# Optimization experiments

Measured on AMD Instinct MI355X. Metric: run time of the kernel, lower is better.

## Reference

```python
import jax, jax.numpy as jnp
import numpy as np

T = 1024
D = 2048
H = 16
NOPE = 128
ROPE = 64
VDIM = 128
QKD = NOPE + ROPE
Q_LORA = 768
KV_LORA = 512
IH = 32          # indexer heads
ID = 128         # indexer head dim (== fp8 quant group size)
TOPK = 256       # indexer top-k sparse selection
E = 8
MOE_K = 2
F = 1024
SH_F = 1024
EPS = 1e-6
FP8_MAX = 448.0
ROUTED_SCALE = 2.5
NEG = jnp.float32(-1e30)


def rms_norm(x, w):
    return x * jax.lax.rsqrt(jnp.mean(jnp.square(x), -1, keepdims=True) + EPS) * w


def layer_norm(x, w, b):
    m = jnp.mean(x, -1, keepdims=True)
    v = jnp.mean(jnp.square(x - m), -1, keepdims=True)
    return (x - m) * jax.lax.rsqrt(v + EPS) * w + b


def rope(x, positions, rope_dim):
    # interleaved (GPT-J style, as DeepSeek MLA uses is_neox_style=False); x: [T, Hx, rope_dim]
    half = rope_dim // 2
    inv_freq = 1.0 / (10000.0 ** (jnp.arange(half, dtype=jnp.float32) / half))
    ang = positions.astype(jnp.float32)[:, None] * inv_freq        # [T, half]
    cos = jnp.cos(ang)[:, None, :]
    sin = jnp.sin(ang)[:, None, :]
    x1, x2 = x[..., ::2], x[..., 1::2]
    return jnp.stack([x1 * cos - x2 * sin, x2 * cos + x1 * sin], -1).reshape(x.shape)


def fp8_quant(x):
    # per-token-group (group = last dim = 128) fp8 e4m3 quant with ue8m0 (power-of-2) scales
    amax = jnp.max(jnp.abs(x), -1, keepdims=True)
    scale = jnp.exp2(jnp.ceil(jnp.log2(jnp.maximum(amax / FP8_MAX, 1e-10))))
    q = jnp.clip(x / scale, -FP8_MAX, FP8_MAX).astype(jnp.float8_e4m3fn).astype(jnp.float32)
    return q, scale


def _forward(positions, hidden_states, residual, input_ln_w, post_ln_w, w_qkv_a, q_a_ln_w,
             w_q_b, kv_a_ln_w, w_kv_b, w_o, w_idx_q_b, w_idx_k, idx_k_ln_w, idx_k_ln_b,
             w_idx_weights, w_gate, w_moe_gate, w_moe_up, w_moe_down, w_sh_gate, w_sh_up, w_sh_down):
    t = hidden_states.shape[0]
    # fused_add_rms_norm
    resid = hidden_states + residual
    hs = rms_norm(resid, input_ln_w)

    # fused qkv_a projection and splits
    qkv = hs @ w_qkv_a                                   # [t, Q_LORA + KV_LORA + ROPE]
    q_c = rms_norm(qkv[:, :Q_LORA], q_a_ln_w)
    kv_c = qkv[:, Q_LORA:Q_LORA + KV_LORA]
    k_pe = qkv[:, Q_LORA + KV_LORA:]
    q = (q_c @ w_q_b).reshape(t, H, QKD)
    kv_c_n = rms_norm(kv_c, kv_a_ln_w)
    q_pe = rope(q[..., NOPE:], positions, ROPE)
    k_pe = rope(k_pe[:, None, :], positions, ROPE)       # [t, 1, ROPE]
    q = jnp.concatenate([q[..., :NOPE], q_pe], -1)

    # lightning indexer: RoPE-split q/k, fp8 per-token-group quant, weighted ReLU scores, top-k
    iq = (q_c @ w_idx_q_b).reshape(t, IH, ID)
    ik = layer_norm(hs @ w_idx_k, idx_k_ln_w, idx_k_ln_b)  # [t, ID]
    iq_pe = rope(iq[..., :ROPE], positions, ROPE)
    ik_pe = rope(ik[:, None, :ROPE], positions, ROPE)[:, 0]
    iq = jnp.concatenate([iq_pe, iq[..., ROPE:]], -1)
    ik = jnp.concatenate([ik_pe, ik[:, ROPE:]], -1)
    iq_fp8, iq_scale = fp8_quant(iq.reshape(t * IH, ID))
    iq_fp8 = iq_fp8.reshape(t, IH, ID)
    iq_scale = iq_scale.reshape(t, IH)
    ik_fp8, ik_scale = fp8_quant(ik)
    # weights_proj * q_scale * softmax_scale * n_heads^-0.5
    iw = (hs @ w_idx_weights) * iq_scale * (ID ** -0.5) * (IH ** -0.5)
    logits = jnp.einsum('thd,sd->ths', iq_fp8, ik_fp8) * ik_scale[:, 0][None, None, :]
    causal = jnp.arange(t)[:, None] >= jnp.arange(t)[None, :]
    scores = jnp.einsum('ths,th->ts', jax.nn.relu(logits), iw)
    scores = jnp.where(causal, scores, NEG)
    topk_idx = jax.lax.top_k(scores, TOPK)[1]            # [t, TOPK]
    sel = jnp.zeros((t, t), bool).at[jnp.arange(t)[:, None], topk_idx].set(True)
    mask = causal & sel

    # MLA attention restricted to indexer-selected tokens
    kv = (kv_c_n @ w_kv_b).reshape(t, H, NOPE + VDIM)
    k = jnp.concatenate([kv[..., :NOPE], jnp.broadcast_to(k_pe, (t, H, ROPE))], -1)
    att = jnp.einsum('thd,shd->hts', q, k) * (QKD ** -0.5)
    att = jnp.where(mask[None], att, NEG)
    p = jax.nn.softmax(att, -1)
    o = jnp.einsum('hts,shv->thv', p, kv[..., NOPE:]).reshape(t, H * VDIM)

    # o_proj + fused_add_rms_norm
    resid = o @ w_o + resid
    hs = rms_norm(resid, post_ln_w)

    # MoE: sigmoid gate, top-k normalized, routed_scaling, SwiGLU experts + shared expert
    gate = jax.nn.sigmoid(hs @ w_gate)                   # [t, E]
    tw, ti = jax.lax.top_k(gate, MOE_K)
    tw = tw / jnp.sum(tw, -1, keepdims=True)
    wfull = jnp.zeros((t, E)).at[jnp.arange(t)[:, None], ti].set(tw) * ROUTED_SCALE
    hmid = jax.nn.silu(jnp.einsum('td,edf->tef', hs, w_moe_gate)) * jnp.einsum('td,edf->tef', hs, w_moe_up)
    routed = jnp.einsum('tef,efd,te->td', hmid, w_moe_down, wfull)
    shared = (jax.nn.silu(hs @ w_sh_gate) * (hs @ w_sh_up)) @ w_sh_down
    return routed + shared, resid


def setup_inputs() -> dict:
    key = jax.random.key(0)
    ks = jax.random.split(key, 16)
    s = 0.02
    return {
        'positions': jnp.arange(T, dtype=jnp.int32),
        'hidden_states': jax.random.normal(ks[0], (T, D), jnp.float32),
        'residual': jax.random.normal(ks[1], (T, D), jnp.float32),
        'input_ln_w': jnp.ones((D,), jnp.float32),
        'post_ln_w': jnp.ones((D,), jnp.float32),
        'w_qkv_a': s * jax.random.normal(ks[2], (D, Q_LORA + KV_LORA + ROPE), jnp.float32),
        'q_a_ln_w': jnp.ones((Q_LORA,), jnp.float32),
        'w_q_b': s * jax.random.normal(ks[3], (Q_LORA, H * QKD), jnp.float32),
        'kv_a_ln_w': jnp.ones((KV_LORA,), jnp.float32),
        'w_kv_b': s * jax.random.normal(ks[4], (KV_LORA, H * (NOPE + VDIM)), jnp.float32),
        'w_o': s * jax.random.normal(ks[5], (H * VDIM, D), jnp.float32),
        'w_idx_q_b': s * jax.random.normal(ks[6], (Q_LORA, IH * ID), jnp.float32),
        'w_idx_k': s * jax.random.normal(ks[7], (D, ID), jnp.float32),
        'idx_k_ln_w': jnp.ones((ID,), jnp.float32),
        'idx_k_ln_b': jnp.zeros((ID,), jnp.float32),
        'w_idx_weights': s * jax.random.normal(ks[8], (D, IH), jnp.float32),
        'w_gate': s * jax.random.normal(ks[9], (D, E), jnp.float32),
        'w_moe_gate': s * jax.random.normal(ks[10], (E, D, F), jnp.float32),
        'w_moe_up': s * jax.random.normal(ks[11], (E, D, F), jnp.float32),
        'w_moe_down': s * jax.random.normal(ks[12], (E, F, D), jnp.float32),
        'w_sh_gate': s * jax.random.normal(ks[13], (D, SH_F), jnp.float32),
        'w_sh_up': s * jax.random.normal(ks[14], (D, SH_F), jnp.float32),
        'w_sh_down': s * jax.random.normal(ks[15], (SH_F, D), jnp.float32),
    }


def reference(positions, hidden_states, residual, input_ln_w, post_ln_w, w_qkv_a, q_a_ln_w,
              w_q_b, kv_a_ln_w, w_kv_b, w_o, w_idx_q_b, w_idx_k, idx_k_ln_w, idx_k_ln_b,
              w_idx_weights, w_gate, w_moe_gate, w_moe_up, w_moe_down, w_sh_gate, w_sh_up, w_sh_down):
    return _forward(positions, hidden_states, residual, input_ln_w, post_ln_w, w_qkv_a, q_a_ln_w,
                    w_q_b, kv_a_ln_w, w_kv_b, w_o, w_idx_q_b, w_idx_k, idx_k_ln_w, idx_k_ln_b,
                    w_idx_weights, w_gate, w_moe_gate, w_moe_up, w_moe_down, w_sh_gate, w_sh_up, w_sh_down)
```

## Files before the change

### kernel.cpp

```cpp
#include <hip/hip_runtime.h>

namespace {
constexpr int kT = 1024, kD = 2048, kH = 16, kNOPE = 128, kROPE = 64, kVD = 128, kQKD = 192;
constexpr int kQL = 768, kKVL = 512, kIH = 32, kID = 128, kTOPK = 256, kE = 8, kF = 1024;
constexpr int kQKV_N = kQL + kKVL + kROPE;
constexpr int kQKV_NP = 1408;
}

typedef __attribute__((ext_vector_type(4))) float floatx4;
typedef __attribute__((ext_vector_type(8))) short short8;
typedef unsigned short u16;

__device__ __forceinline__ float wsum(float v) {
#pragma unroll
  for (int o = 32; o; o >>= 1) v += __shfl_xor(v, o, 64);
  return v;
}
__device__ __forceinline__ float wmax64(float v) {
#pragma unroll
  for (int o = 32; o; o >>= 1) v = fmaxf(v, __shfl_xor(v, o, 64));
  return v;
}
__device__ __forceinline__ int wsum_i(int v) {
#pragma unroll
  for (int o = 32; o; o >>= 1) v += __shfl_xor(v, o, 64);
  return v;
}
__device__ __forceinline__ float bsum256(float v, float* red) {
  v = wsum(v);
  if ((threadIdx.x & 63) == 0) red[threadIdx.x >> 6] = v;
  __syncthreads();
  float t = red[0] + red[1] + red[2] + red[3];
  __syncthreads();
  return t;
}
__device__ __forceinline__ unsigned sortkey(float f) {
  unsigned b = __float_as_uint(f);
  return (b & 0x80000000u) ? ~b : (b | 0x80000000u);
}
__device__ __forceinline__ float pow2ceil(float z) {
  unsigned b = __float_as_uint(z);
  if ((b & 0x7FFFFFu) == 0) return z;
  return __uint_as_float((((b >> 23) & 0xFFu) + 1u) << 23);
}
__device__ __forceinline__ float fp8q(float x) {
  float ax = fabsf(x);
  float q;
  if (ax < 0.015625f) {
    q = rintf(ax * 512.0f) * 0.001953125f;
  } else {
    unsigned b = __float_as_uint(ax);
    int e = (int)((b >> 23) & 0xFF) - 127;
    float quant = __uint_as_float((unsigned)(e - 3 + 127) << 23);
    float rq    = __uint_as_float((unsigned)(127 - (e - 3)) << 23);
    q = rintf(ax * rq) * quant;
  }
  return copysignf(q, x);
}
__device__ __forceinline__ u16 f2bf(float x) {
  unsigned u = __float_as_uint(x);
  u += 0x7FFFu + ((u >> 16) & 1u);
  return (u16)(u >> 16);
}
__device__ __forceinline__ float bf2f(u16 h) { return __uint_as_float((unsigned)h << 16); }

__device__ __forceinline__ void gld_lds16(const void* g, void* l) {
  __builtin_amdgcn_global_load_lds(
      (const __attribute__((address_space(1))) unsigned int*)(unsigned long long)g,
      (__attribute__((address_space(3))) unsigned int*)(unsigned int)(unsigned long long)l,
      16, 0, 0);
}
__device__ __forceinline__ void stage_tile(const u16* g, size_t strideUs, u16* tile, int wave, int lane) {
  int r = lane >> 2, c = lane & 3;
  const u16* gp = g + (size_t)(wave * 32 + r) * strideUs + c * 8;
  gld_lds16(gp, tile + (wave * 32) * 32);
  gld_lds16(gp + (size_t)16 * strideUs, tile + (wave * 32 + 16) * 32);
}

__global__ __launch_bounds__(256) void k_transpose_w(const float* __restrict__ in, u16* __restrict__ hi,
                                                     u16* __restrict__ lo, int K, int N, int Npad) {
  __shared__ float tile[32][33];
  int n0 = blockIdx.x * 32, k0 = blockIdx.y * 32;
  const float* ip = in + (size_t)blockIdx.z * K * N;
  u16* hp = hi + (size_t)blockIdx.z * Npad * K;
  u16* lp = lo ? lo + (size_t)blockIdx.z * Npad * K : nullptr;
  int t = threadIdx.x;
  int r = t >> 3, c4 = (t & 7) << 2;
  if (n0 < N) {
    float4 v = *(const float4*)&ip[(size_t)(k0 + r) * N + n0 + c4];
    tile[r][c4] = v.x; tile[r][c4 + 1] = v.y; tile[r][c4 + 2] = v.z; tile[r][c4 + 3] = v.w;
  } else {
    tile[r][c4] = 0.f; tile[r][c4 + 1] = 0.f; tile[r][c4 + 2] = 0.f; tile[r][c4 + 3] = 0.f;
  }
  __syncthreads();
  int n = t >> 3, kq = (t & 7) << 2;
  ushort4 h4, l4;
#pragma unroll
  for (int j = 0; j < 4; j++) {
    float f = tile[kq + j][n];
    u16 h = f2bf(f);
    ((u16*)&h4)[j] = h;
    ((u16*)&l4)[j] = f2bf(f - bf2f(h));
  }
  *(ushort4*)&hp[(size_t)(n0 + n) * K + k0 + kq] = h4;
  if (lp) *(ushort4*)&lp[(size_t)(n0 + n) * K + k0 + kq] = l4;
}


__global__ __launch_bounds__(256) void k_gemm_bt(const u16* __restrict__ A, const u16* __restrict__ BT,
                                                 float* __restrict__ C, const float* __restrict__ addend,
                                                 int M, int N, int K) {
  __shared__ __align__(16) u16 As[128 * 32];
  __shared__ __align__(16) u16 Bs[128 * 32];
  int tid = threadIdx.x, wave = tid >> 6, lane = tid & 63;
  int bm = blockIdx.y * 128, bn = blockIdx.x * 128;
  int wy = (wave >> 1) * 64, wx = (wave & 1) * 64;
  int lm = lane & 15, lk = lane >> 4;
  const u16* Ab = A + (size_t)bm * K;
  const u16* Bb = BT + (size_t)bn * K;
  floatx4 acc[4][4] = {};
  for (int k0 = 0; k0 < K; k0 += 32) {
    stage_tile(Ab + k0, K, As, wave, lane);
    stage_tile(Bb + k0, K, Bs, wave, lane);
    __syncthreads();
    short8 af[4], bfr[4];
#pragma unroll
    for (int mt = 0; mt < 4; mt++) af[mt] = *(short8*)&As[(wy + mt * 16 + lm) * 32 + lk * 8];
#pragma unroll
    for (int nt = 0; nt < 4; nt++) bfr[nt] = *(short8*)&Bs[(wx + nt * 16 + lm) * 32 + lk * 8];
#pragma unroll
    for (int mt = 0; mt < 4; mt++)
#pragma unroll
      for (int nt = 0; nt < 4; nt++)
        acc[mt][nt] = __builtin_amdgcn_mfma_f32_16x16x32_bf16(af[mt], bfr[nt], acc[mt][nt], 0, 0, 0);
    __syncthreads();
  }
#pragma unroll
  for (int mt = 0; mt < 4; mt++)
#pragma unroll
    for (int nt = 0; nt < 4; nt++)
#pragma unroll
      for (int r = 0; r < 4; r++) {
        int m = bm + wy + mt * 16 + lk * 4 + r;
        int n = bn + wx + nt * 16 + lm;
        float v = acc[mt][nt][r];
        if (addend) v += addend[(size_t)m * N + n];
        C[(size_t)m * N + n] = v;
      }
}

__global__ __launch_bounds__(256) void k_gemm_split(const u16* __restrict__ Ah, const u16* __restrict__ Al,
                                                    const u16* __restrict__ Bh, const u16* __restrict__ Bl,
                                                    float* __restrict__ C, int M, int N, int K) {
  __shared__ __align__(16) u16 Ahs[128 * 32];
  __shared__ __align__(16) u16 Als[128 * 32];
  __shared__ __align__(16) u16 Bhs[128 * 32];
  __shared__ __align__(16) u16 Bls[128 * 32];
  int tid = threadIdx.x, wave = tid >> 6, lane = tid & 63;
  int bm = blockIdx.y * 128, bn = blockIdx.x * 128;
  int wy = (wave >> 1) * 64, wx = (wave & 1) * 64;
  int lm = lane & 15, lk = lane >> 4;
  floatx4 acc[4][4] = {};
  for (int k0 = 0; k0 < K; k0 += 32) {
    stage_tile(Ah + (size_t)bm * K + k0, K, Ahs, wave, lane);
    stage_tile(Al + (size_t)bm * K + k0, K, Als, wave, lane);
    stage_tile(Bh + (size_t)bn * K + k0, K, Bhs, wave, lane);
    stage_tile(Bl + (size_t)bn * K + k0, K, Bls, wave, lane);
    __syncthreads();
    short8 ah[4], al[4], bh[4], bl[4];
#pragma unroll
    for (int mt = 0; mt < 4; mt++) { ah[mt] = *(short8*)&Ahs[(wy + mt * 16 + lm) * 32 + lk * 8];
                                     al[mt] = *(short8*)&Als[(wy + mt * 16 + lm) * 32 + lk * 8]; }
#pragma unroll
    for (int nt = 0; nt < 4; nt++) { bh[nt] = *(short8*)&Bhs[(wx + nt * 16 + lm) * 32 + lk * 8];
                                     bl[nt] = *(short8*)&Bls[(wx + nt * 16 + lm) * 32 + lk * 8]; }
#pragma unroll
    for (int mt = 0; mt < 4; mt++)
#pragma unroll
      for (int nt = 0; nt < 4; nt++) {
        floatx4 a = acc[mt][nt];
        a = __builtin_amdgcn_mfma_f32_16x16x32_bf16(al[mt], bh[nt], a, 0, 0, 0);
        a = __builtin_amdgcn_mfma_f32_16x16x32_bf16(ah[mt], bl[nt], a, 0, 0, 0);
        a = __builtin_amdgcn_mfma_f32_16x16x32_bf16(ah[mt], bh[nt], a, 0, 0, 0);
        acc[mt][nt] = a;
      }
    __syncthreads();
  }
#pragma unroll
  for (int mt = 0; mt < 4; mt++)
#pragma unroll
    for (int nt = 0; nt < 4; nt++)
#pragma unroll
      for (int r = 0; r < 4; r++) {
        int m = bm + wy + mt * 16 + lk * 4 + r;
        int n = bn + wx + nt * 16 + lm;
        if (n < N) C[(size_t)m * N + n] = acc[mt][nt][r];
      }
}

__global__ __launch_bounds__(256) void k_dual_bt(const u16* __restrict__ A, const u16* __restrict__ GT,
                                                 const u16* __restrict__ UT, u16* __restrict__ out,
                                                 const int* __restrict__ toki, const int* __restrict__ cnt,
                                                 int M, int N, int K) {
  int e = blockIdx.z;
  int n_rows = toki ? cnt[e] : M;
  int bm = blockIdx.y * 128;
  if (bm >= n_rows) return;
  int bn = blockIdx.x * 128;
  const int* tk = toki ? (toki + e * kT) : nullptr;
  const u16* Gb = GT + (size_t)e * N * K + (size_t)bn * K;
  const u16* Ub = UT + (size_t)e * N * K + (size_t)bn * K;
  u16* oP = out + (size_t)e * kT * N;
  __shared__ __align__(16) u16 As[128 * 32];
  __shared__ __align__(16) u16 Gs[128 * 32];
  __shared__ __align__(16) u16 Us[128 * 32];
  int tid = threadIdx.x, wave = tid >> 6, lane = tid & 63;
  int wy = (wave >> 1) * 64, wx = (wave & 1) * 64;
  int lm = lane & 15, lk = lane >> 4;
  int r = lane >> 2, c = lane & 3;
  int r0 = bm + wave * 32 + r, r1 = r0 + 16;
  size_t arow0 = tk ? (size_t)((r0 < n_rows) ? tk[r0] : 0) : (size_t)r0;
  size_t arow1 = tk ? (size_t)((r1 < n_rows) ? tk[r1] : 0) : (size_t)r1;
  floatx4 ag[4][4] = {}, au[4][4] = {};
  for (int k0 = 0; k0 < K; k0 += 32) {
    gld_lds16(A + arow0 * K + k0 + c * 8, As + (wave * 32) * 32);
    gld_lds16(A + arow1 * K + k0 + c * 8, As + (wave * 32 + 16) * 32);
    stage_tile(Gb + k0, K, Gs, wave, lane);
    stage_tile(Ub + k0, K, Us, wave, lane);
    __syncthreads();
    short8 af[4], gf[4], uf[4];
#pragma unroll
    for (int mt = 0; mt < 4; mt++) af[mt] = *(short8*)&As[(wy + mt * 16 + lm) * 32 + lk * 8];
#pragma unroll
    for (int nt = 0; nt < 4; nt++) { gf[nt] = *(short8*)&Gs[(wx + nt * 16 + lm) * 32 + lk * 8];
                                     uf[nt] = *(short8*)&Us[(wx + nt * 16 + lm) * 32 + lk * 8]; }
#pragma unroll
    for (int mt = 0; mt < 4; mt++)
#pragma unroll
      for (int nt = 0; nt < 4; nt++) {
        ag[mt][nt] = __builtin_amdgcn_mfma_f32_16x16x32_bf16(af[mt], gf[nt], ag[mt][nt], 0, 0, 0);
        au[mt][nt] = __builtin_amdgcn_mfma_f32_16x16x32_bf16(af[mt], uf[nt], au[mt][nt], 0, 0, 0);
      }
    __syncthreads();
  }
#pragma unroll
  for (int mt = 0; mt < 4; mt++)
#pragma unroll
    for (int nt = 0; nt < 4; nt++)
#pragma unroll
      for (int r2 = 0; r2 < 4; r2++) {
        int gm = bm + wy + mt * 16 + lk * 4 + r2;
        if (gm >= n_rows) continue;
        int n = bn + wx + nt * 16 + lm;
        float gv = ag[mt][nt][r2], uv = au[mt][nt][r2];
        oP[(size_t)gm * N + n] = f2bf(gv * (1.0f / (1.0f + expf(-gv))) * uv);
      }
}

__global__ __launch_bounds__(256) void k_down_bt(const u16* __restrict__ hmid, const u16* __restrict__ DT,
                                                 const int* __restrict__ toki, const float* __restrict__ tokw,
                                                 const int* __restrict__ cnt, float* __restrict__ out) {
  int e = blockIdx.z;
  int n_rows = cnt[e];
  int bm = blockIdx.y * 128;
  if (bm >= n_rows) return;
  int bn = blockIdx.x * 128;
  const u16* Ab = hmid + (size_t)e * kT * kF + (size_t)bm * kF;
  const u16* Bb = DT + (size_t)e * kD * kF + (size_t)bn * kF;
  __shared__ __align__(16) u16 As[128 * 32];
  __shared__ __align__(16) u16 Bs[128 * 32];
  int tid = threadIdx.x, wave = tid >> 6, lane = tid & 63;
  int wy = (wave >> 1) * 64, wx = (wave & 1) * 64;
  int lm = lane & 15, lk = lane >> 4;
  floatx4 acc[4][4] = {};
  for (int k0 = 0; k0 < kF; k0 += 32) {
    stage_tile(Ab + k0, kF, As, wave, lane);
    stage_tile(Bb + k0, kF, Bs, wave, lane);
    __syncthreads();
    short8 af[4], bfr[4];
#pragma unroll
    for (int mt = 0; mt < 4; mt++) af[mt] = *(short8*)&As[(wy + mt * 16 + lm) * 32 + lk * 8];
#pragma unroll
    for (int nt = 0; nt < 4; nt++) bfr[nt] = *(short8*)&Bs[(wx + nt * 16 + lm) * 32 + lk * 8];
#pragma unroll
    for (int mt = 0; mt < 4; mt++)
#pragma unroll
      for (int nt = 0; nt < 4; nt++)
        acc[mt][nt] = __builtin_amdgcn_mfma_f32_16x16x32_bf16(af[mt], bfr[nt], acc[mt][nt], 0, 0, 0);
    __syncthreads();
  }
#pragma unroll
  for (int mt = 0; mt < 4; mt++)
#pragma unroll
    for (int r = 0; r < 4; r++) {
      int gm = bm + wy + mt * 16 + lk * 4 + r;
      if (gm >= n_rows) continue;
      int tt = toki[e * kT + gm];
      float w = tokw[e * kT + gm];
#pragma unroll
      for (int nt = 0; nt < 4; nt++) {
        int n = bn + wx + nt * 16 + lm;
        atomicAdd(&out[(size_t)tt * kD + n], w * acc[mt][nt][r]);
      }
    }
}

__global__ __launch_bounds__(256) void k_attn_mfma(const float* __restrict__ q, const float* __restrict__ kv,
                                                   const float* __restrict__ kpe,
                                                   const unsigned long long* __restrict__ mbits,
                                                   u16* __restrict__ o) {
  __shared__ __align__(16) u16 Ks[64 * 200];
  __shared__ __align__(16) u16 Vs[128 * 72];
  __shared__ __align__(16) u16 Ps[4 * 16 * 72];
  int h = blockIdx.y;
  int qb = gridDim.x - 1 - blockIdx.x;
  int qbase = qb * 64;
  int tid = threadIdx.x;
  int wave = tid >> 6, lane = tid & 63;
  int lm = lane & 15, lk = lane >> 4;
  short8 qf[6];
  {
    const float* qrow = q + ((size_t)(qbase + wave * 16 + lm) * kH + h) * kQKD;
#pragma unroll
    for (int ks = 0; ks < 6; ks++) {
      const float4 a0 = *(const float4*)&qrow[ks * 32 + lk * 8];
      const float4 a1 = *(const float4*)&qrow[ks * 32 + lk * 8 + 4];
      short8 f;
      f[0] = (short)f2bf(a0.x); f[1] = (short)f2bf(a0.y); f[2] = (short)f2bf(a0.z); f[3] = (short)f2bf(a0.w);
      f[4] = (short)f2bf(a1.x); f[5] = (short)f2bf(a1.y); f[6] = (short)f2bf(a1.z); f[7] = (short)f2bf(a1.w);
      qf[ks] = f;
    }
  }
  float m_r[4] = {-1e30f, -1e30f, -1e30f, -1e30f};
  float l_r[4] = {};
  floatx4 Oacc[8] = {};
  int sr = tid >> 2, sj = tid & 3;
  int nch = qb + 1;
  for (int ch = 0; ch < nch; ch++) {
    int s0 = ch << 6;
    __syncthreads();
    {
      const float* kvrow = kv + ((size_t)(s0 + sr) * kH + h) * 256;
      const float* kprow = kpe + (size_t)(s0 + sr) * 64;
#pragma unroll
      for (int i = 0; i < 12; i++) {
        int c4 = (i << 2) + sj;
        float4 v4 = (c4 < 32) ? *(const float4*)&kvrow[c4 * 4] : *(const float4*)&kprow[(c4 - 32) * 4];
        ushort4 p; p.x = f2bf(v4.x); p.y = f2bf(v4.y); p.z = f2bf(v4.z); p.w = f2bf(v4.w);
        *(ushort4*)&Ks[sr * 200 + c4 * 4] = p;
      }
      const float* vrow = kvrow + 128;
#pragma unroll
      for (int i = 0; i < 8; i++) {
        int c4 = (i << 2) + sj;
        float4 v4 = *(const float4*)&vrow[c4 * 4];
        Vs[(c4 * 4 + 0) * 72 + sr] = f2bf(v4.x);
        Vs[(c4 * 4 + 1) * 72 + sr] = f2bf(v4.y);
        Vs[(c4 * 4 + 2) * 72 + sr] = f2bf(v4.z);
        Vs[(c4 * 4 + 3) * 72 + sr] = f2bf(v4.w);
      }
    }
    __syncthreads();
    floatx4 sacc[4] = {};
#pragma unroll
    for (int ks = 0; ks < 6; ks++) {
      short8 kf[4];
#pragma unroll
      for (int nt = 0; nt < 4; nt++) kf[nt] = *(short8*)&Ks[(nt * 16 + lm) * 200 + ks * 32 + lk * 8];
#pragma unroll
      for (int nt = 0; nt < 4; nt++)
        sacc[nt] = __builtin_amdgcn_mfma_f32_16x16x32_bf16(qf[ks], kf[nt], sacc[nt], 0, 0, 0);
    }
    unsigned long long mw[4];
#pragma unroll
    for (int r = 0; r < 4; r++) mw[r] = mbits[(size_t)(qbase + wave * 16 + lk * 4 + r) * 16 + ch];
    float mx[4] = {-1e30f, -1e30f, -1e30f, -1e30f};
#pragma unroll
    for (int nt = 0; nt < 4; nt++)
#pragma unroll
      for (int r = 0; r < 4; r++) {
        int sel = (int)((mw[r] >> (nt * 16 + lm)) & 1ull);
        float sv = sel ? sacc[nt][r] * 0.07216878364870323f : -1e30f;
        sacc[nt][r] = sv;
        mx[r] = fmaxf(mx[r], sv);
      }
#pragma unroll
    for (int off = 1; off < 16; off <<= 1)
#pragma unroll
      for (int r = 0; r < 4; r++) mx[r] = fmaxf(mx[r], __shfl_xor(mx[r], off, 64));
    float al[4], psum[4] = {};
#pragma unroll
    for (int r = 0; r < 4; r++) {
      float mnew = fmaxf(m_r[r], mx[r]);
      al[r] = __expf(m_r[r] - mnew);
      m_r[r] = mnew;
    }
#pragma unroll
    for (int nt = 0; nt < 4; nt++)
#pragma unroll
      for (int r = 0; r < 4; r++) {
        float p = (sacc[nt][r] > -0.9e30f) ? __expf(sacc[nt][r] - m_r[r]) : 0.0f;
        psum[r] += p;
        Ps[wave * 1152 + (lk * 4 + r) * 72 + nt * 16 + lm] = f2bf(p);
      }
#pragma unroll
    for (int off = 1; off < 16; off <<= 1)
#pragma unroll
      for (int r = 0; r < 4; r++) psum[r] += __shfl_xor(psum[r], off, 64);
#pragma unroll
    for (int r = 0; r < 4; r++) l_r[r] = l_r[r] * al[r] + psum[r];
#pragma unroll
    for (int nv = 0; nv < 8; nv++)
#pragma unroll
      for (int r = 0; r < 4; r++) Oacc[nv][r] *= al[r];
    short8 pf[2];
#pragma unroll
    for (int k2 = 0; k2 < 2; k2++) pf[k2] = *(short8*)&Ps[wave * 1152 + lm * 72 + k2 * 32 + lk * 8];
#pragma unroll
    for (int k2 = 0; k2 < 2; k2++)
#pragma unroll
      for (int nv = 0; nv < 8; nv++) {
        short8 vf = *(short8*)&Vs[(nv * 16 + lm) * 72 + k2 * 32 + lk * 8];
        Oacc[nv] = __builtin_amdgcn_mfma_f32_16x16x32_bf16(pf[k2], vf, Oacc[nv], 0, 0, 0);
      }
  }
  float invl[4];
#pragma unroll
  for (int r = 0; r < 4; r++) invl[r] = 1.0f / l_r[r];
#pragma unroll
  for (int nv = 0; nv < 8; nv++)
#pragma unroll
    for (int r = 0; r < 4; r++) {
      int t_row = qbase + wave * 16 + lk * 4 + r;
      o[((size_t)t_row * kH + h) * kVD + nv * 16 + lm] = f2bf(Oacc[nv][r] * invl[r]);
    }
}

__global__ __launch_bounds__(256) void k_add_rms(const float* __restrict__ h, const float* __restrict__ r,
                                                 const float* __restrict__ w, float* __restrict__ resid,
                                                 float* __restrict__ out, u16* __restrict__ oh,
                                                 u16* __restrict__ ol) {
  __shared__ float row[kD];
  __shared__ float red[4];
  int t = blockIdx.x;
  size_t base = (size_t)t * kD;
  float ss = 0.f;
  for (int c = threadIdx.x; c < kD; c += 256) {
    float v = h[base + c] + r[base + c];
    row[c] = v; resid[base + c] = v; ss += v * v;
  }
  float tot = bsum256(ss, red);
  float inv = 1.0f / sqrtf(tot * (1.0f / kD) + 1e-6f);
  for (int c = threadIdx.x; c < kD; c += 256) {
    float v = row[c] * inv * w[c];
    out[base + c] = v;
    u16 hb = f2bf(v);
    oh[base + c] = hb;
    ol[base + c] = f2bf(v - bf2f(hb));
  }
}

__global__ __launch_bounds__(256) void k_rms_rows(const float* __restrict__ in, int stride, int off,
                                                  const float* __restrict__ w, float* __restrict__ outf,
                                                  u16* __restrict__ oh, u16* __restrict__ ol, int cols) {
  __shared__ float row[kD];
  __shared__ float red[4];
  int t = blockIdx.x;
  const float* x = in + (size_t)t * stride + off;
  float ss = 0.f;
  for (int c = threadIdx.x; c < cols; c += 256) { float v = x[c]; row[c] = v; ss += v * v; }
  float tot = bsum256(ss, red);
  float inv = 1.0f / sqrtf(tot / (float)cols + 1e-6f);
  for (int c = threadIdx.x; c < cols; c += 256) {
    float v = row[c] * inv * w[c];
    if (outf) outf[(size_t)t * cols + c] = v;
    if (oh) {
      u16 hb = f2bf(v);
      oh[(size_t)t * cols + c] = hb;
      if (ol) ol[(size_t)t * cols + c] = f2bf(v - bf2f(hb));
    }
  }
}

__global__ __launch_bounds__(256) void k_iw_fused(const float* __restrict__ hs, const float* __restrict__ w,
                                                  const float* __restrict__ iqsc, float* __restrict__ out) {
  __shared__ float red[4][32];
  int t = blockIdx.x;
  int tid = threadIdx.x;
  int h = tid & 31, g = tid >> 5;
  const float* hrow = hs + (size_t)t * kD;
  float acc = 0.f;
#pragma unroll 4
  for (int d = g; d < kD; d += 8) acc += hrow[d] * w[(size_t)d * kIH + h];
  acc += __shfl_xor(acc, 32, 64);
  int wave = tid >> 6, lane = tid & 63;
  if (lane < 32) red[wave][lane] = acc;
  __syncthreads();
  if (tid < 32) {
    float v = red[0][tid] + red[1][tid] + red[2][tid] + red[3][tid];
    out[t * kIH + tid] = v * iqsc[t * kIH + tid] * 0.08838834764831845f * 0.17677669529663687f;
  }
}

__global__ __launch_bounds__(256) void k_rope_q(float* __restrict__ q, const int* __restrict__ pos) {
  int t = blockIdx.x;
  float p = (float)pos[t];
  for (int idx = threadIdx.x; idx < kH * 32; idx += 256) {
    int h = idx >> 5, j = idx & 31;
    float invf = 1.0f / powf(10000.0f, (float)j * 0.03125f);
    float ang = p * invf; float s, c; sincosf(ang, &s, &c);
    size_t base = ((size_t)t * kH + h) * kQKD + kNOPE + 2 * j;
    float x1 = q[base], x2 = q[base + 1];
    q[base] = x1 * c - x2 * s;
    q[base + 1] = x2 * c + x1 * s;
  }
}

__global__ __launch_bounds__(256) void k_rope_iq(float* __restrict__ iq, const int* __restrict__ pos) {
  int t = blockIdx.x;
  float p = (float)pos[t];
  for (int idx = threadIdx.x; idx < kIH * 32; idx += 256) {
    int h = idx >> 5, j = idx & 31;
    float invf = 1.0f / powf(10000.0f, (float)j * 0.03125f);
    float ang = p * invf; float s, c; sincosf(ang, &s, &c);
    size_t base = ((size_t)t * kIH + h) * kID + 2 * j;
    float x1 = iq[base], x2 = iq[base + 1];
    iq[base] = x1 * c - x2 * s;
    iq[base + 1] = x2 * c + x1 * s;
  }
}

__global__ __launch_bounds__(64) void k_rope_kpe(const float* __restrict__ qkv, const int* __restrict__ pos,
                                                 float* __restrict__ kpe) {
  int t = blockIdx.x; int j = threadIdx.x;
  if (j >= 32) return;
  float p = (float)pos[t];
  float invf = 1.0f / powf(10000.0f, (float)j * 0.03125f);
  float ang = p * invf; float s, c; sincosf(ang, &s, &c);
  const float* src = qkv + (size_t)t * kQKV_N + kQL + kKVL;
  float x1 = src[2 * j], x2 = src[2 * j + 1];
  kpe[(size_t)t * 64 + 2 * j] = x1 * c - x2 * s;
  kpe[(size_t)t * 64 + 2 * j + 1] = x2 * c + x1 * s;
}

__global__ __launch_bounds__(64) void k_quant_rows(const float* __restrict__ x, u16* __restrict__ outq,
                                                   float* __restrict__ scales) {
  int row = blockIdx.x;
  const float* p = x + (size_t)row * kID;
  int l = threadIdx.x;
  float v0 = p[2 * l], v1 = p[2 * l + 1];
  float am = wmax64(fmaxf(fabsf(v0), fabsf(v1)));
  float scale = pow2ceil(fmaxf(am / 448.0f, 1e-10f));
  float inv = 1.0f / scale;
  float q0 = fp8q(fminf(fmaxf(v0 * inv, -448.f), 448.f));
  float q1 = fp8q(fminf(fmaxf(v1 * inv, -448.f), 448.f));
  ushort2 pk; pk.x = f2bf(q0); pk.y = f2bf(q1);
  *(ushort2*)&outq[(size_t)row * kID + 2 * l] = pk;
  if (l == 0) scales[row] = scale;
}

__global__ __launch_bounds__(64) void k_ik_process(const float* __restrict__ raw, const float* __restrict__ w,
                                                   const float* __restrict__ b, const int* __restrict__ pos,
                                                   u16* __restrict__ outq, float* __restrict__ scales) {
  int t = blockIdx.x; int l = threadIdx.x;
  const float* x = raw + (size_t)t * kID;
  float x0 = x[2 * l], x1 = x[2 * l + 1];
  float mean = wsum(x0 + x1) * (1.0f / 128.0f);
  float d0 = x0 - mean, d1 = x1 - mean;
  float var = wsum(d0 * d0 + d1 * d1) * (1.0f / 128.0f);
  float inv = 1.0f / sqrtf(var + 1e-6f);
  float y0 = d0 * inv * w[2 * l] + b[2 * l];
  float y1 = d1 * inv * w[2 * l + 1] + b[2 * l + 1];
  if (l < 32) {
    float p = (float)pos[t];
    float invf = 1.0f / powf(10000.0f, (float)l * 0.03125f);
    float ang = p * invf; float sn, cs; sincosf(ang, &sn, &cs);
    float r0 = y0 * cs - y1 * sn, r1 = y1 * cs + y0 * sn;
    y0 = r0; y1 = r1;
  }
  float am = wmax64(fmaxf(fabsf(y0), fabsf(y1)));
  float scale = pow2ceil(fmaxf(am / 448.0f, 1e-10f));
  float is = 1.0f / scale;
  float q0 = fp8q(fminf(fmaxf(y0 * is, -448.f), 448.f));
  float q1 = fp8q(fminf(fmaxf(y1 * is, -448.f), 448.f));
  ushort2 pk; pk.x = f2bf(q0); pk.y = f2bf(q1);
  *(ushort2*)&outq[(size_t)t * kID + 2 * l] = pk;
  if (l == 0) scales[t] = scale;
}

__global__ __launch_bounds__(256) void k_scores_mfma(const u16* __restrict__ iq, const u16* __restrict__ ik,
                                                     const float* __restrict__ iksc, const float* __restrict__ iw,
                                                     float* __restrict__ scores) {
  int tb = blockIdx.y * 4;
  int bn = blockIdx.x * 128;
  if (bn > tb + 3) return;
  __shared__ __align__(16) u16 As[128 * 32];
  __shared__ __align__(16) u16 Bs[128 * 32];
  int tid = threadIdx.x, wave = tid >> 6, lane = tid & 63;
  int wy = (wave >> 1) * 64, wx = (wave & 1) * 64;
  int lm = lane & 15, lk = lane >> 4;
  const u16* Ab = iq + (size_t)(tb * kIH) * kID;
  const u16* Bb = ik + (size_t)bn * kID;
  floatx4 acc[4][4] = {};
  for (int k0 = 0; k0 < kID; k0 += 32) {
    stage_tile(Ab + k0, kID, As, wave, lane);
    stage_tile(Bb + k0, kID, Bs, wave, lane);
    __syncthreads();
    short8 af[4], bfr[4];
#pragma unroll
    for (int mt = 0; mt < 4; mt++) af[mt] = *(short8*)&As[(wy + mt * 16 + lm) * 32 + lk * 8];
#pragma unroll
    for (int nt = 0; nt < 4; nt++) bfr[nt] = *(short8*)&Bs[(wx + nt * 16 + lm) * 32 + lk * 8];
#pragma unroll
    for (int mt = 0; mt < 4; mt++)
#pragma unroll
      for (int nt = 0; nt < 4; nt++)
        acc[mt][nt] = __builtin_amdgcn_mfma_f32_16x16x32_bf16(af[mt], bfr[nt], acc[mt][nt], 0, 0, 0);
    __syncthreads();
  }
  float scv[4];
#pragma unroll
  for (int nt = 0; nt < 4; nt++) scv[nt] = iksc[bn + wx + nt * 16 + lm];
  float iwv[4][4];
#pragma unroll
  for (int mt = 0; mt < 4; mt++)
#pragma unroll
    for (int r = 0; r < 4; r++)
      iwv[mt][r] = iw[(tb + (wy >> 5) + (mt >> 1)) * kIH + (mt & 1) * 16 + lk * 4 + r];
#pragma unroll
  for (int tp = 0; tp < 2; tp++) {
    int tglob = tb + (wy >> 5) + tp;
#pragma unroll
    for (int nt = 0; nt < 4; nt++) {
      float v = 0.f;
#pragma unroll
      for (int mh = 0; mh < 2; mh++) {
        int mt = tp * 2 + mh;
#pragma unroll
        for (int r = 0; r < 4; r++)
          v += fmaxf(acc[mt][nt][r] * scv[nt], 0.f) * iwv[mt][r];
      }
      v += __shfl_xor(v, 16, 64);
      v += __shfl_xor(v, 32, 64);
      if (lk == 0) scores[(size_t)tglob * kT + bn + wx + nt * 16 + lm] = v;
    }
  }
}

__global__ __launch_bounds__(64) void k_topk(const float* __restrict__ scores, unsigned long long* __restrict__ mbits) {
  int t = blockIdx.x; int l = threadIdx.x;
  __shared__ unsigned short tmp[64];
  unsigned long long* mrow = mbits + (size_t)t * 16;
  if (t < kTOPK) {
    if (l < 16) {
      int lo = l * 64, hi = lo + 63;
      unsigned long long bits;
      if (hi <= t) bits = ~0ull;
      else if (lo > t) bits = 0ull;
      else bits = (1ull << (t - lo + 1)) - 1ull;
      mrow[l] = bits;
    }
    return;
  }
  unsigned key[16];
  const float* srow = scores + (size_t)t * kT;
#pragma unroll
  for (int i = 0; i < 16; i++) {
    int s = l * 16 + i;
    key[i] = (s <= t) ? sortkey(srow[s]) : 0u;
  }
  unsigned prefix = 0; int remaining = kTOPK;
  for (int bit = 31; bit >= 0; bit--) {
    unsigned himask = 0xFFFFFFFFu << bit;
    unsigned cmp = prefix | (1u << bit);
    int c = 0;
#pragma unroll
    for (int i = 0; i < 16; i++) c += ((key[i] & himask) == cmp) ? 1 : 0;
    c = wsum_i(c);
    if (c >= remaining) prefix = cmp; else remaining -= c;
  }
  int ceq = 0, cgt = 0;
#pragma unroll
  for (int i = 0; i < 16; i++) { ceq += (key[i] == prefix) ? 1 : 0; cgt += (key[i] > prefix) ? 1 : 0; }
  int v = ceq;
#pragma unroll
  for (int o = 1; o < 64; o <<= 1) { int u = __shfl_up(v, o, 64); if (l >= o) v += u; }
  int rank = v - ceq;
  int need = kTOPK - wsum_i(cgt);
  unsigned short mybits = 0;
#pragma unroll
  for (int i = 0; i < 16; i++) {
    int sel;
    if (key[i] > prefix) sel = 1;
    else if (key[i] == prefix) { sel = (rank < need) ? 1 : 0; rank++; }
    else sel = 0;
    mybits |= (unsigned short)(sel << i);
  }
  tmp[l] = mybits;
  __syncthreads();
  if (l < 16) {
    mrow[l] = (unsigned long long)tmp[4 * l] | ((unsigned long long)tmp[4 * l + 1] << 16) |
              ((unsigned long long)tmp[4 * l + 2] << 32) | ((unsigned long long)tmp[4 * l + 3] << 48);
  }
}

__global__ __launch_bounds__(64) void k_route(const float* __restrict__ hs2, const float* __restrict__ wg,
                                              int* __restrict__ cnt, int* __restrict__ toki,
                                              float* __restrict__ tokw) {
  int t = blockIdx.x; int l = threadIdx.x;
  float acc[8] = {};
  for (int d = l; d < kD; d += 64) {
    float hv = hs2[(size_t)t * kD + d];
    const float* wr = wg + (size_t)d * 8;
#pragma unroll
    for (int e = 0; e < 8; e++) acc[e] += hv * wr[e];
  }
#pragma unroll
  for (int e = 0; e < 8; e++) acc[e] = wsum(acc[e]);
  if (l == 0) {
    float g[8];
#pragma unroll
    for (int e = 0; e < 8; e++) g[e] = 1.0f / (1.0f + expf(-acc[e]));
    int i0 = 0;
    for (int e = 1; e < 8; e++) if (g[e] > g[i0]) i0 = e;
    int i1 = (i0 == 0) ? 1 : 0;
    for (int e = 0; e < 8; e++) if (e != i0 && g[e] > g[i1]) i1 = e;
    float ssum = g[i0] + g[i1];
    float w0 = g[i0] / ssum * 2.5f, w1 = g[i1] / ssum * 2.5f;
    int s0 = atomicAdd(&cnt[i0], 1); toki[i0 * kT + s0] = t; tokw[i0 * kT + s0] = w0;
    int s1 = atomicAdd(&cnt[i1], 1); toki[i1 * kT + s1] = t; tokw[i1 * kT + s1] = w1;
  }
}

extern "C" void kernel_launch(void* const* d_in, const int* in_sizes, int n_in,
                              void* d_out, int out_size, void* d_ws, size_t ws_size,
                              hipStream_t stream) {
  (void)in_sizes; (void)n_in; (void)out_size; (void)ws_size;
  const int*   positions  = (const int*)d_in[0];
  const float* hidden     = (const float*)d_in[1];
  const float* residual   = (const float*)d_in[2];
  const float* input_ln_w = (const float*)d_in[3];
  const float* post_ln_w  = (const float*)d_in[4];
  const float* w_qkv_a    = (const float*)d_in[5];
  const float* q_a_ln_w   = (const float*)d_in[6];
  const float* w_q_b      = (const float*)d_in[7];
  const float* kv_a_ln_w  = (const float*)d_in[8];
  const float* w_kv_b     = (const float*)d_in[9];
  const float* w_o        = (const float*)d_in[10];
  const float* w_idx_q_b  = (const float*)d_in[11];
  const float* w_idx_k    = (const float*)d_in[12];
  const float* idx_k_ln_w = (const float*)d_in[13];
  const float* idx_k_ln_b = (const float*)d_in[14];
  const float* w_idx_w    = (const float*)d_in[15];
  const float* w_gate     = (const float*)d_in[16];
  const float* w_moe_gate = (const float*)d_in[17];
  const float* w_moe_up   = (const float*)d_in[18];
  const float* w_moe_down = (const float*)d_in[19];
  const float* w_sh_gate  = (const float*)d_in[20];
  const float* w_sh_up    = (const float*)d_in[21];
  const float* w_sh_down  = (const float*)d_in[22];

  float* out0 = (float*)d_out;
  float* out1 = out0 + (size_t)kT * kD;

  char* W = (char*)d_ws;
  size_t off = 0;
  auto alloc = [&](size_t bytes) { char* p = W + off; off += (bytes + 255) & ~(size_t)255; return p; };
  float* resid   = (float*)alloc((size_t)kT * kD * 4);
  float* hs      = (float*)alloc((size_t)kT * kD * 4);
  float* qkv     = (float*)alloc((size_t)kT * kQKV_N * 4);
  float* qb      = (float*)alloc((size_t)kT * kH * kQKD * 4);
  float* kvb     = (float*)alloc((size_t)kT * kH * 256 * 4);
  float* iqb     = (float*)alloc((size_t)kT * kIH * kID * 4);
  float* ikraw   = (float*)alloc((size_t)kT * kID * 4);
  float* iksc    = (float*)alloc(kT * 4);
  float* iqsc    = (float*)alloc((size_t)kT * kIH * 4);
  float* iwb     = (float*)alloc((size_t)kT * kIH * 4);
  float* kpe     = (float*)alloc((size_t)kT * kROPE * 4);
  float* scoresb = (float*)alloc((size_t)kT * kT * 4);
  float* hs2     = (float*)alloc((size_t)kT * kD * 4);
  unsigned long long* mbits = (unsigned long long*)alloc((size_t)kT * 16 * 8);
  float* tokw    = (float*)alloc((size_t)kE * kT * 4);
  int*   toki    = (int*)alloc((size_t)kE * kT * 4);
  int*   cnt     = (int*)alloc(64);
  u16* hs_h   = (u16*)alloc((size_t)kT * kD * 2);
  u16* hs_l   = (u16*)alloc((size_t)kT * kD * 2);
  u16* qc_h   = (u16*)alloc((size_t)kT * kQL * 2);
  u16* qc_l   = (u16*)alloc((size_t)kT * kQL * 2);
  u16* kvc_h  = (u16*)alloc((size_t)kT * kKVL * 2);
  u16* o_bf   = (u16*)alloc((size_t)kT * kH * kVD * 2);
  u16* hs2_h  = (u16*)alloc((size_t)kT * kD * 2);
  u16* sg_bf  = (u16*)alloc((size_t)kT * kF * 2);
  u16* hmid_bf= (u16*)alloc((size_t)kE * kT * kF * 2);
  u16* iq_bf  = (u16*)alloc((size_t)kT * kIH * kID * 2);
  u16* ik_bf  = (u16*)alloc((size_t)kT * kID * 2);
  u16* qkvBT_h = (u16*)alloc((size_t)kQKV_NP * kD * 2);
  u16* qkvBT_l = (u16*)alloc((size_t)kQKV_NP * kD * 2);
  u16* qbBT    = (u16*)alloc((size_t)kH * kQKD * kQL * 2);
  u16* kvbBT   = (u16*)alloc((size_t)kH * 256 * kKVL * 2);
  u16* woBT    = (u16*)alloc((size_t)kD * kH * kVD * 2);
  u16* iqBT_h  = (u16*)alloc((size_t)kIH * kID * kQL * 2);
  u16* iqBT_l  = (u16*)alloc((size_t)kIH * kID * kQL * 2);
  u16* ikBT_h  = (u16*)alloc((size_t)kID * kD * 2);
  u16* ikBT_l  = (u16*)alloc((size_t)kID * kD * 2);
  u16* shgBT   = (u16*)alloc((size_t)kF * kD * 2);
  u16* shuBT   = (u16*)alloc((size_t)kF * kD * 2);
  u16* shdBT   = (u16*)alloc((size_t)kD * kF * 2);
  u16* moegBT  = (u16*)alloc((size_t)kE * kF * kD * 2);
  u16* moeuBT  = (u16*)alloc((size_t)kE * kF * kD * 2);
  u16* moedBT  = (u16*)alloc((size_t)kE * kD * kF * 2);

  { dim3 g(kQKV_NP / 32, kD / 32); k_transpose_w<<<g, 256, 0, stream>>>(w_qkv_a, qkvBT_h, qkvBT_l, kD, kQKV_N, kQKV_NP); }
  { dim3 g(kH * kQKD / 32, kQL / 32); k_transpose_w<<<g, 256, 0, stream>>>(w_q_b, qbBT, nullptr, kQL, kH * kQKD, kH * kQKD); }
  { dim3 g(kH * 256 / 32, kKVL / 32); k_transpose_w<<<g, 256, 0, stream>>>(w_kv_b, kvbBT, nullptr, kKVL, kH * 256, kH * 256); }
  { dim3 g(kD / 32, kH * kVD / 32); k_transpose_w<<<g, 256, 0, stream>>>(w_o, woBT, nullptr, kH * kVD, kD, kD); }
  { dim3 g(kIH * kID / 32, kQL / 32); k_transpose_w<<<g, 256, 0, stream>>>(w_idx_q_b, iqBT_h, iqBT_l, kQL, kIH * kID, kIH * kID); }
  { dim3 g(kID / 32, kD / 32); k_transpose_w<<<g, 256, 0, stream>>>(w_idx_k, ikBT_h, ikBT_l, kD, kID, kID); }
  { dim3 g(kF / 32, kD / 32); k_transpose_w<<<g, 256, 0, stream>>>(w_sh_gate, shgBT, nullptr, kD, kF, kF); }
  { dim3 g(kF / 32, kD / 32); k_transpose_w<<<g, 256, 0, stream>>>(w_sh_up, shuBT, nullptr, kD, kF, kF); }
  { dim3 g(kD / 32, kF / 32); k_transpose_w<<<g, 256, 0, stream>>>(w_sh_down, shdBT, nullptr, kF, kD, kD); }
  { dim3 g(kF / 32, kD / 32, kE); k_transpose_w<<<g, 256, 0, stream>>>(w_moe_gate, moegBT, nullptr, kD, kF, kF); }
  { dim3 g(kF / 32, kD / 32, kE); k_transpose_w<<<g, 256, 0, stream>>>(w_moe_up, moeuBT, nullptr, kD, kF, kF); }
  { dim3 g(kD / 32, kF / 32, kE); k_transpose_w<<<g, 256, 0, stream>>>(w_moe_down, moedBT, nullptr, kF, kD, kD); }

  k_add_rms<<<kT, 256, 0, stream>>>(hidden, residual, input_ln_w, resid, hs, hs_h, hs_l);
  { dim3 g(kQKV_NP / 128, kT / 128); k_gemm_split<<<g, 256, 0, stream>>>(hs_h, hs_l, qkvBT_h, qkvBT_l, qkv, kT, kQKV_N, kD); }
  k_rms_rows<<<kT, 256, 0, stream>>>(qkv, kQKV_N, 0, q_a_ln_w, nullptr, qc_h, qc_l, kQL);
  k_rms_rows<<<kT, 256, 0, stream>>>(qkv, kQKV_N, kQL, kv_a_ln_w, nullptr, kvc_h, nullptr, kKVL);
  { dim3 g(kH * kQKD / 128, kT / 128); k_gemm_bt<<<g, 256, 0, stream>>>(qc_h, qbBT, qb, nullptr, kT, kH * kQKD, kQL); }
  { dim3 g(kIH * kID / 128, kT / 128); k_gemm_split<<<g, 256, 0, stream>>>(qc_h, qc_l, iqBT_h, iqBT_l, iqb, kT, kIH * kID, kQL); }
  { dim3 g(kH * 256 / 128, kT / 128); k_gemm_bt<<<g, 256, 0, stream>>>(kvc_h, kvbBT, kvb, nullptr, kT, kH * 256, kKVL); }
  { dim3 g(kID / 128, kT / 128); k_gemm_split<<<g, 256, 0, stream>>>(hs_h, hs_l, ikBT_h, ikBT_l, ikraw, kT, kID, kD); }
  k_rope_q<<<kT, 256, 0, stream>>>(qb, positions);
  k_rope_iq<<<kT, 256, 0, stream>>>(iqb, positions);
  k_rope_kpe<<<kT, 64, 0, stream>>>(qkv, positions, kpe);
  k_quant_rows<<<kT * kIH, 64, 0, stream>>>(iqb, iq_bf, iqsc);
  k_ik_process<<<kT, 64, 0, stream>>>(ikraw, idx_k_ln_w, idx_k_ln_b, positions, ik_bf, iksc);
  k_iw_fused<<<kT, 256, 0, stream>>>(hs, w_idx_w, iqsc, iwb);
  { dim3 g(kT / 128, kT / 4); k_scores_mfma<<<g, 256, 0, stream>>>(iq_bf, ik_bf, iksc, iwb, scoresb); }
  k_topk<<<kT, 64, 0, stream>>>(scoresb, mbits);
  { dim3 g(kT / 64, kH); k_attn_mfma<<<g, 256, 0, stream>>>(qb, kvb, kpe, mbits, o_bf); }
  { dim3 g(kD / 128, kT / 128); k_gemm_bt<<<g, 256, 0, stream>>>(o_bf, woBT, out1, resid, kT, kD, kH * kVD); }
  k_rms_rows<<<kT, 256, 0, stream>>>(out1, kD, 0, post_ln_w, hs2, hs2_h, nullptr, kD);
  hipMemsetAsync(cnt, 0, 8 * sizeof(int), stream);
  k_route<<<kT, 64, 0, stream>>>(hs2, w_gate, cnt, toki, tokw);
  { dim3 g(kF / 128, kT / 128, 1); k_dual_bt<<<g, 256, 0, stream>>>(hs2_h, shgBT, shuBT, sg_bf, nullptr, nullptr, kT, kF, kD); }
  { dim3 g(kD / 128, kT / 128); k_gemm_bt<<<g, 256, 0, stream>>>(sg_bf, shdBT, out0, nullptr, kT, kD, kF); }
  { dim3 g(kF / 128, kT / 128, kE); k_dual_bt<<<g, 256, 0, stream>>>(hs2_h, moegBT, moeuBT, hmid_bf, toki, cnt, kT, kF, kD); }
  { dim3 g(kD / 128, kT / 128, kE); k_down_bt<<<g, 256, 0, stream>>>(hmid_bf, moedBT, toki, tokw, cnt, out0); }
}
```

Before: 1.148 ms.

## Fuse indexer-k projection into qkv_a GEMM and split K four ways

Appends the indexer key weight to the padded qkv_a weight matrix so one GEMM computes both projections. That GEMM is split along K into four chunks writing partial sums to a scratch buffer (aliased onto kvb), then reduced by a separate vectorized kernel. The split is meant to raise block count for a small-N, long-K GEMM (12x8 tiles otherwise) and drop one launch, at the cost of extra partial-sum traffic and a reduction pass. Padding columns between 1344 and 1408 become zero-weight work.

Result: faster. 1.005 ms (-12.4%).

```diff
diff --git a/kernel.cpp b/kernel.cpp
--- a/kernel.cpp
+++ b/kernel.cpp
@@ -5,6 +5,8 @@
 constexpr int kQL = 768, kKVL = 512, kIH = 32, kID = 128, kTOPK = 256, kE = 8, kF = 1024;
 constexpr int kQKV_N = kQL + kKVL + kROPE;
 constexpr int kQKV_NP = 1408;
+constexpr int kIKOFF = 1408;
+constexpr int kQKV_F = 1536;
 }
 
 typedef __attribute__((ext_vector_type(4))) float floatx4;
@@ -196,6 +198,66 @@
         int n = bn + wx + nt * 16 + lm;
         if (n < N) C[(size_t)m * N + n] = acc[mt][nt][r];
       }
+}
+
+__global__ __launch_bounds__(256) void k_gemm_splitk(const u16* __restrict__ Ah, const u16* __restrict__ Al,
+                                                     const u16* __restrict__ Bh, const u16* __restrict__ Bl,
+                                                     float* __restrict__ Cp, int M, int Npad, int K, int kchunk) {
+  __shared__ __align__(16) u16 Ahs[128 * 32];
+  __shared__ __align__(16) u16 Als[128 * 32];
+  __shared__ __align__(16) u16 Bhs[128 * 32];
+  __shared__ __align__(16) u16 Bls[128 * 32];
+  int tid = threadIdx.x, wave = tid >> 6, lane = tid & 63;
+  int bm = blockIdx.y * 128, bn = blockIdx.x * 128;
+  int kz = blockIdx.z;
+  int kbeg = kz * kchunk, kend = kbeg + kchunk;
+  int wy = (wave >> 1) * 64, wx = (wave & 1) * 64;
+  int lm = lane & 15, lk = lane >> 4;
+  floatx4 acc[4][4] = {};
+  for (int k0 = kbeg; k0 < kend; k0 += 32) {
+    stage_tile(Ah + (size_t)bm * K + k0, K, Ahs, wave, lane);
+    stage_tile(Al + (size_t)bm * K + k0, K, Als, wave, lane);
+    stage_tile(Bh + (size_t)bn * K + k0, K, Bhs, wave, lane);
+    stage_tile(Bl + (size_t)bn * K + k0, K, Bls, wave, lane);
+    __syncthreads();
+    short8 ah[4], al[4], bh[4], bl[4];
+#pragma unroll
+    for (int mt = 0; mt < 4; mt++) { ah[mt] = *(short8*)&Ahs[(wy + mt * 16 + lm) * 32 + lk * 8];
+                                     al[mt] = *(short8*)&Als[(wy + mt * 16 + lm) * 32 + lk * 8]; }
+#pragma unroll
+    for (int nt = 0; nt < 4; nt++) { bh[nt] = *(short8*)&Bhs[(wx + nt * 16 + lm) * 32 + lk * 8];
+                                     bl[nt] = *(short8*)&Bls[(wx + nt * 16 + lm) * 32 + lk * 8]; }
+#pragma unroll
+    for (int mt = 0; mt < 4; mt++)
+#pragma unroll
+      for (int nt = 0; nt < 4; nt++) {
+        floatx4 a = acc[mt][nt];
+        a = __builtin_amdgcn_mfma_f32_16x16x32_bf16(al[mt], bh[nt], a, 0, 0, 0);
+        a = __builtin_amdgcn_mfma_f32_16x16x32_bf16(ah[mt], bl[nt], a, 0, 0, 0);
+        a = __builtin_amdgcn_mfma_f32_16x16x32_bf16(ah[mt], bh[nt], a, 0, 0, 0);
+        acc[mt][nt] = a;
+      }
+    __syncthreads();
+  }
+  float* Co = Cp + (size_t)kz * M * Npad;
+#pragma unroll
+  for (int mt = 0; mt < 4; mt++)
+#pragma unroll
+    for (int nt = 0; nt < 4; nt++)
+#pragma unroll
+      for (int r = 0; r < 4; r++) {
+        int m = bm + wy + mt * 16 + lk * 4 + r;
+        int n = bn + wx + nt * 16 + lm;
+        Co[(size_t)m * Npad + n] = acc[mt][nt][r];
+      }
+}
+
+__global__ __launch_bounds__(256) void k_reduce4(const float* __restrict__ Cp, float* __restrict__ C, int n4) {
+  int i = blockIdx.x * 256 + threadIdx.x;
+  if (i >= n4) return;
+  const floatx4* p = (const floatx4*)Cp;
+  floatx4 v = p[i] + p[i + n4] + p[i + 2 * n4] + p[i + 3 * n4];
+  ((floatx4*)C)[i] = v;
 }
 
 __global__ __launch_bounds__(256) void k_dual_bt(const u16* __restrict__ A, const u16* __restrict__ GT,
@@ -530,14 +592,14 @@
   }
 }
 
-__global__ __launch_bounds__(64) void k_rope_kpe(const float* __restrict__ qkv, const int* __restrict__ pos,
-                                                 float* __restrict__ kpe) {
+__global__ __launch_bounds__(64) void k_rope_kpe(const float* __restrict__ qkv, int stride,
+                                                 const int* __restrict__ pos, float* __restrict__ kpe) {
   int t = blockIdx.x; int j = threadIdx.x;
   if (j >= 32) return;
   float p = (float)pos[t];
   float invf = 1.0f / powf(10000.0f, (float)j * 0.03125f);
   float ang = p * invf; float s, c; sincosf(ang, &s, &c);
-  const float* src = qkv + (size_t)t * kQKV_N + kQL + kKVL;
+  const float* src = qkv + (size_t)t * stride + kQL + kKVL;
   float x1 = src[2 * j], x2 = src[2 * j + 1];
   kpe[(size_t)t * 64 + 2 * j] = x1 * c - x2 * s;
   kpe[(size_t)t * 64 + 2 * j + 1] = x2 * c + x1 * s;
@@ -559,11 +621,12 @@
   if (l == 0) scales[row] = scale;
 }
 
-__global__ __launch_bounds__(64) void k_ik_process(const float* __restrict__ raw, const float* __restrict__ w,
+__global__ __launch_bounds__(64) void k_ik_process(const float* __restrict__ raw, int stride,
+                                                   const float* __restrict__ w,
                                                    const float* __restrict__ b, const int* __restrict__ pos,
                                                    u16* __restrict__ outq, float* __restrict__ scales) {
   int t = blockIdx.x; int l = threadIdx.x;
-  const float* x = raw + (size_t)t * kID;
+  const float* x = raw + (size_t)t * stride;
   float x0 = x[2 * l], x1 = x[2 * l + 1];
   float mean = wsum(x0 + x1) * (1.0f / 128.0f);
   float d0 = x0 - mean, d1 = x1 - mean;
@@ -768,11 +831,10 @@
   auto alloc = [&](size_t bytes) { char* p = W + off; off += (bytes + 255) & ~(size_t)255; return p; };
   float* resid   = (float*)alloc((size_t)kT * kD * 4);
   float* hs      = (float*)alloc((size_t)kT * kD * 4);
-  float* qkv     = (float*)alloc((size_t)kT * kQKV_N * 4);
+  float* qkvF    = (float*)alloc((size_t)kT * kQKV_F * 4);
   float* qb      = (float*)alloc((size_t)kT * kH * kQKD * 4);
   float* kvb     = (float*)alloc((size_t)kT * kH * 256 * 4);
   float* iqb     = (float*)alloc((size_t)kT * kIH * kID * 4);
-  float* ikraw   = (float*)alloc((size_t)kT * kID * 4);
   float* iksc    = (float*)alloc(kT * 4);
   float* iqsc    = (float*)alloc((size_t)kT * kIH * 4);
   float* iwb     = (float*)alloc((size_t)kT * kIH * 4);
@@ -783,6 +845,7 @@
   float* tokw    = (float*)alloc((size_t)kE * kT * 4);
   int*   toki    = (int*)alloc((size_t)kE * kT * 4);
   int*   cnt     = (int*)alloc(64);
+  float* qkvP    = kvb;
   u16* hs_h   = (u16*)alloc((size_t)kT * kD * 2);
   u16* hs_l   = (u16*)alloc((size_t)kT * kD * 2);
   u16* qc_h   = (u16*)alloc((size_t)kT * kQL * 2);
@@ -794,15 +857,13 @@
   u16* hmid_bf= (u16*)alloc((size_t)kE * kT * kF * 2);
   u16* iq_bf  = (u16*)alloc((size_t)kT * kIH * kID * 2);
   u16* ik_bf  = (u16*)alloc((size_t)kT * kID * 2);
-  u16* qkvBT_h = (u16*)alloc((size_t)kQKV_NP * kD * 2);
-  u16* qkvBT_l = (u16*)alloc((size_t)kQKV_NP * kD * 2);
+  u16* qkvBT_h = (u16*)alloc((size_t)kQKV_F * kD * 2);
+  u16* qkvBT_l = (u16*)alloc((size_t)kQKV_F * kD * 2);
   u16* qbBT    = (u16*)alloc((size_t)kH * kQKD * kQL * 2);
   u16* kvbBT   = (u16*)alloc((size_t)kH * 256 * kKVL * 2);
   u16* woBT    = (u16*)alloc((size_t)kD * kH * kVD * 2);
   u16* iqBT_h  = (u16*)alloc((size_t)kIH * kID * kQL * 2);
   u16* iqBT_l  = (u16*)alloc((size_t)kIH * kID * kQL * 2);
-  u16* ikBT_h  = (u16*)alloc((size_t)kID * kD * 2);
-  u16* ikBT_l  = (u16*)alloc((size_t)kID * kD * 2);
   u16* shgBT   = (u16*)alloc((size_t)kF * kD * 2);
   u16* shuBT   = (u16*)alloc((size_t)kF * kD * 2);
   u16* shdBT   = (u16*)alloc((size_t)kD * kF * 2);
@@ -811,11 +872,11 @@
   u16* moedBT  = (u16*)alloc((size_t)kE * kD * kF * 2);
 
   { dim3 g(kQKV_NP / 32, kD / 32); k_transpose_w<<<g, 256, 0, stream>>>(w_qkv_a, qkvBT_h, qkvBT_l, kD, kQKV_N, kQKV_NP); }
+  { dim3 g(kID / 32, kD / 32); k_transpose_w<<<g, 256, 0, stream>>>(w_idx_k, qkvBT_h + (size_t)kIKOFF * kD, qkvBT_l + (size_t)kIKOFF * kD, kD, kID, kID); }
   { dim3 g(kH * kQKD / 32, kQL / 32); k_transpose_w<<<g, 256, 0, stream>>>(w_q_b, qbBT, nullptr, kQL, kH * kQKD, kH * kQKD); }
   { dim3 g(kH * 256 / 32, kKVL / 32); k_transpose_w<<<g, 256, 0, stream>>>(w_kv_b, kvbBT, nullptr, kKVL, kH * 256, kH * 256); }
   { dim3 g(kD / 32, kH * kVD / 32); k_transpose_w<<<g, 256, 0, stream>>>(w_o, woBT, nullptr, kH * kVD, kD, kD); }
   { dim3 g(kIH * kID / 32, kQL / 32); k_transpose_w<<<g, 256, 0, stream>>>(w_idx_q_b, iqBT_h, iqBT_l, kQL, kIH * kID, kIH * kID); }
-  { dim3 g(kID / 32, kD / 32); k_transpose_w<<<g, 256, 0, stream>>>(w_idx_k, ikBT_h, ikBT_l, kD, kID, kID); }
   { dim3 g(kF / 32, kD / 32); k_transpose_w<<<g, 256, 0, stream>>>(w_sh_gate, shgBT, nullptr, kD, kF, kF); }
   { dim3 g(kF / 32, kD / 32); k_transpose_w<<<g, 256, 0, stream>>>(w_sh_up, shuBT, nullptr, kD, kF, kF); }
   { dim3 g(kD / 32, kF / 32); k_transpose_w<<<g, 256, 0, stream>>>(w_sh_down, shdBT, nullptr, kF, kD, kD); }
@@ -824,18 +885,18 @@
   { dim3 g(kD / 32, kF / 32, kE); k_transpose_w<<<g, 256, 0, stream>>>(w_moe_down, moedBT, nullptr, kF, kD, kD); }
 
   k_add_rms<<<kT, 256, 0, stream>>>(hidden, residual, input_ln_w, resid, hs, hs_h, hs_l);
-  { dim3 g(kQKV_NP / 128, kT / 128); k_gemm_split<<<g, 256, 0, stream>>>(hs_h, hs_l, qkvBT_h, qkvBT_l, qkv, kT, kQKV_N, kD); }
-  k_rms_rows<<<kT, 256, 0, stream>>>(qkv, kQKV_N, 0, q_a_ln_w, nullptr, qc_h, qc_l, kQL);
-  k_rms_rows<<<kT, 256, 0, stream>>>(qkv, kQKV_N, kQL, kv_a_ln_w, nullptr, kvc_h, nullptr, kKVL);
+  { dim3 g(kQKV_F / 128, kT / 128, 4); k_gemm_splitk<<<g, 256, 0, stream>>>(hs_h, hs_l, qkvBT_h, qkvBT_l, qkvP, kT, kQKV_F, kD, kD / 4); }
+  { int n4 = kT * kQKV_F / 4; k_reduce4<<<(n4 + 255) / 256, 256, 0, stream>>>(qkvP, qkvF, n4); }
+  k_rms_rows<<<kT, 256, 0, stream>>>(qkvF, kQKV_F, 0, q_a_ln_w, nullptr, qc_h, qc_l, kQL);
+  k_rms_rows<<<kT, 256, 0, stream>>>(qkvF, kQKV_F, kQL, kv_a_ln_w, nullptr, kvc_h, nullptr, kKVL);
   { dim3 g(kH * kQKD / 128, kT / 128); k_gemm_bt<<<g, 256, 0, stream>>>(qc_h, qbBT, qb, nullptr, kT, kH * kQKD, kQL); }
   { dim3 g(kIH * kID / 128, kT / 128); k_gemm_split<<<g, 256, 0, stream>>>(qc_h, qc_l, iqBT_h, iqBT_l, iqb, kT, kIH * kID, kQL); }
   { dim3 g(kH * 256 / 128, kT / 128); k_gemm_bt<<<g, 256, 0, stream>>>(kvc_h, kvbBT, kvb, nullptr, kT, kH * 256, kKVL); }
-  { dim3 g(kID / 128, kT / 128); k_gemm_split<<<g, 256, 0, stream>>>(hs_h, hs_l, ikBT_h, ikBT_l, ikraw, kT, kID, kD); }
   k_rope_q<<<kT, 256, 0, stream>>>(qb, positions);
   k_rope_iq<<<kT, 256, 0, stream>>>(iqb, positions);
-  k_rope_kpe<<<kT, 64, 0, stream>>>(qkv, positions, kpe);
+  k_rope_kpe<<<kT, 64, 0, stream>>>(qkvF, kQKV_F, positions, kpe);
   k_quant_rows<<<kT * kIH, 64, 0, stream>>>(iqb, iq_bf, iqsc);
-  k_ik_process<<<kT, 64, 0, stream>>>(ikraw, idx_k_ln_w, idx_k_ln_b, positions, ik_bf, iksc);
+  k_ik_process<<<kT, 64, 0, stream>>>(qkvF + kIKOFF, kQKV_F, idx_k_ln_w, idx_k_ln_b, positions, ik_bf, iksc);
   k_iw_fused<<<kT, 256, 0, stream>>>(hs, w_idx_w, iqsc, iwb);
   { dim3 g(kT / 128, kT / 4); k_scores_mfma<<<g, 256, 0, stream>>>(iq_bf, ik_bf, iksc, iwb, scoresb); }
   k_topk<<<kT, 64, 0, stream>>>(scoresb, mbits);
```
